# Kernel tuning notes

Hardware: AMD Instinct MI355X
Metric: run time of the kernel (lower is better)

Reference implementation:

```python
import jax, jax.numpy as jnp
import numpy as np

N = 200000   # total nodes across batched graphs
E = 800000   # directed edges (grid graph, avg degree ~4)
G = 8        # number of graphs in the batch
IN_DIM, INTER_DIM, OUT_DIM, LAYER_NUM = 2, 128, 64, 4


def setup_inputs() -> dict:
    key = jax.random.key(0)
    ks = jax.random.split(key, 10)
    x = jax.random.normal(ks[0], (N, IN_DIM), jnp.float32)
    edge_index = jax.random.randint(ks[1], (2, E), 0, N, dtype=jnp.int32)
    batch = jnp.sort(jax.random.randint(ks[2], (N,), 0, G, dtype=jnp.int32))

    def glorot(k, fan_in, fan_out):
        s = (2.0 / (fan_in + fan_out)) ** 0.5
        return jax.random.normal(k, (fan_in, fan_out), jnp.float32) * s

    W_in = glorot(ks[3], IN_DIM, INTER_DIM)
    b_in = jnp.zeros((INTER_DIM,), jnp.float32)
    W_hidden = jnp.stack([glorot(jax.random.fold_in(ks[4], i), INTER_DIM, INTER_DIM)
                          for i in range(LAYER_NUM)])
    b_hidden = jnp.zeros((LAYER_NUM, INTER_DIM), jnp.float32)
    W_out = glorot(ks[5], INTER_DIM, OUT_DIM)
    b_out = jnp.zeros((OUT_DIM,), jnp.float32)
    return {"x": x, "edge_index": edge_index, "batch": batch,
            "W_in": W_in, "b_in": b_in, "W_hidden": W_hidden,
            "b_hidden": b_hidden, "W_out": W_out, "b_out": b_out}


def reference(x, edge_index, batch, W_in, b_in, W_hidden, b_hidden, W_out, b_out):
    num_nodes = x.shape[0]
    loops = jnp.arange(num_nodes, dtype=edge_index.dtype)
    # PyG GCNConv: add self loops, symmetric degree normalization
    src = jnp.concatenate([edge_index[0], loops])
    dst = jnp.concatenate([edge_index[1], loops])
    deg = jax.ops.segment_sum(jnp.ones_like(src, x.dtype), dst, num_segments=num_nodes)
    dinv = jnp.where(deg > 0, jax.lax.rsqrt(jnp.maximum(deg, 1.0)), 0.0)
    norm = dinv[src] * dinv[dst]  # [E+N]

    def gcn_conv(h, W, b):
        m = h @ W                                  # [N, F'] dense transform
        msg = norm[:, None] * m[src]               # gather + scale
        out = jax.ops.segment_sum(msg, dst, num_segments=num_nodes)  # scatter-add
        return out + b

    h = gcn_conv(x, W_in, b_in)
    for i in range(W_hidden.shape[0]):
        h = jax.nn.relu(gcn_conv(h, W_hidden[i], b_hidden[i]))
    h = gcn_conv(h, W_out, b_out)

    # global mean pool over batch assignment, then sigmoid
    sums = jax.ops.segment_sum(h, batch, num_segments=G)
    cnts = jax.ops.segment_sum(jnp.ones((num_nodes,), h.dtype), batch, num_segments=G)
    return jax.nn.sigmoid(sums / jnp.maximum(cnts, 1.0)[:, None])
```

## Files before the change

kernel.cpp:

```cpp
#include <hip/hip_runtime.h>
#include <math.h>

#define INTER 128
#define OUTD  64
#define SCAN_T 256
#define SCAN_E 1024
#define NSLOT 64

using bf16x8 = __attribute__((ext_vector_type(8))) short;
using f32x4  = __attribute__((ext_vector_type(4))) float;

static __device__ __forceinline__ unsigned short f2bf(float f) {
    unsigned int u = __float_as_uint(f);
    u += 0x7fffu + ((u >> 16) & 1u);
    return (unsigned short)(u >> 16);
}
static __device__ __forceinline__ unsigned int pk2(float a, float b) {
    return (unsigned int)f2bf(a) | ((unsigned int)f2bf(b) << 16);
}
static __device__ __forceinline__ float bflo(unsigned int u) { return __uint_as_float(u << 16); }
static __device__ __forceinline__ float bfhi(unsigned int u) { return __uint_as_float(u & 0xffff0000u); }

static __device__ __forceinline__ void fma8(float* a, float w, uint4 v) {
    a[0] = fmaf(w, bflo(v.x), a[0]); a[1] = fmaf(w, bfhi(v.x), a[1]);
    a[2] = fmaf(w, bflo(v.y), a[2]); a[3] = fmaf(w, bfhi(v.y), a[3]);
    a[4] = fmaf(w, bflo(v.z), a[4]); a[5] = fmaf(w, bfhi(v.z), a[5]);
    a[6] = fmaf(w, bflo(v.w), a[6]); a[7] = fmaf(w, bfhi(v.w), a[7]);
}
static __device__ __forceinline__ void seed8(float* a, float sn, uint4 v) {
    a[0] = sn * bflo(v.x); a[1] = sn * bfhi(v.x);
    a[2] = sn * bflo(v.y); a[3] = sn * bfhi(v.y);
    a[4] = sn * bflo(v.z); a[5] = sn * bfhi(v.z);
    a[6] = sn * bflo(v.w); a[7] = sn * bfhi(v.w);
}
static __device__ __forceinline__ void seed4(float* a, float sn, uint2 v) {
    a[0] = sn * bflo(v.x); a[1] = sn * bfhi(v.x);
    a[2] = sn * bflo(v.y); a[3] = sn * bfhi(v.y);
}

__global__ void count_k(const int* __restrict__ dst, int* __restrict__ cnt, int E) {
    int e = blockIdx.x * 256 + threadIdx.x;
    if (e < E) atomicAdd(&cnt[dst[e]], 1);
}

__global__ void dinv_k(const int* __restrict__ cnt, float* __restrict__ dinv, int N) {
    int i = blockIdx.x * 256 + threadIdx.x;
    if (i < N) dinv[i] = rsqrtf((float)(cnt[i] + 1));
}

__global__ void scan_block(const int* __restrict__ in, int* __restrict__ out,
                           int* __restrict__ bsums, int n) {
    __shared__ int sh[SCAN_T];
    int base = blockIdx.x * SCAN_E;
    int t = threadIdx.x;
    int v[4];
    int s = 0;
#pragma unroll
    for (int i = 0; i < 4; i++) {
        int idx = base + t * 4 + i;
        v[i] = (idx < n) ? in[idx] : 0;
        s += v[i];
    }
    sh[t] = s;
    __syncthreads();
    for (int off = 1; off < SCAN_T; off <<= 1) {
        int x = (t >= off) ? sh[t - off] : 0;
        __syncthreads();
        sh[t] += x;
        __syncthreads();
    }
    int excl = (t == 0) ? 0 : sh[t - 1];
    if (bsums && t == SCAN_T - 1) bsums[blockIdx.x] = sh[t];
#pragma unroll
    for (int i = 0; i < 4; i++) {
        int idx = base + t * 4 + i;
        if (idx < n) out[idx] = excl;
        excl += v[i];
    }
}

__global__ void scan_add(int* __restrict__ out, const int* __restrict__ bsums, int n, int total) {
    int idx = blockIdx.x * SCAN_E + threadIdx.x * 4;
    int add = bsums[blockIdx.x];
#pragma unroll
    for (int i = 0; i < 4; i++) {
        int j = idx + i;
        if (j < n) out[j] += add;
    }
    if (blockIdx.x == 0 && threadIdx.x == 0) out[n] = total;
}

__global__ void scatter_k(const int* __restrict__ src, const int* __restrict__ dst,
                          const int* __restrict__ rs, int* __restrict__ cursor,
                          const float* __restrict__ dinv,
                          int2* __restrict__ cw, int E) {
    int e = blockIdx.x * 256 + threadIdx.x;
    if (e >= E) return;
    int s = src[e], d = dst[e];
    int pos = rs[d] + atomicAdd(&cursor[d], 1);
    cw[pos] = make_int2(s, __float_as_int(dinv[s] * dinv[d]));
}

__global__ void wprep_h(const float* __restrict__ W, unsigned short* __restrict__ Wt, int L) {
    int tid = blockIdx.x * 256 + threadIdx.x;
    if (tid >= L * INTER * INTER) return;
    int l = tid / (INTER * INTER);
    int r = tid % (INTER * INTER);
    int n = r / INTER, k = r % INTER;
    Wt[tid] = f2bf(W[(size_t)l * INTER * INTER + (size_t)k * INTER + n]);
}

__global__ void wprep_o(const float* __restrict__ W, unsigned short* __restrict__ Wt) {
    int tid = blockIdx.x * 256 + threadIdx.x;
    if (tid >= OUTD * INTER) return;
    int n = tid / INTER, k = tid % INTER;
    Wt[tid] = f2bf(W[(size_t)k * OUTD + n]);
}

__global__ void agg2(const float* __restrict__ x, const int* __restrict__ rs,
                     const int2* __restrict__ cw, const float* __restrict__ dinv,
                     float* __restrict__ ax, int N) {
    int i = blockIdx.x * 256 + threadIdx.x;
    if (i >= N) return;
    float di = dinv[i];
    float sn = di * di;
    float2 xv = ((const float2*)x)[i];
    float a0 = sn * xv.x, a1 = sn * xv.y;
    int e0 = rs[i], e1 = rs[i + 1];
    for (int k = e0; k < e1; k++) {
        int2 c = cw[k];
        float wk = __int_as_float(c.y);
        float2 xs = ((const float2*)x)[c.x];
        a0 += wk * xs.x;
        a1 += wk * xs.y;
    }
    ((float2*)ax)[i] = make_float2(a0, a1);
}

__global__ void gemm_in(const float* __restrict__ ax, const float* __restrict__ Wi,
                        const float* __restrict__ bi, unsigned short* __restrict__ h, int N) {
    int node = blockIdx.x * 2 + threadIdx.x / 128;
    int j = threadIdx.x % 128;
    if (node >= N) return;
    float2 a = ((const float2*)ax)[node];
    h[(size_t)node * 128 + j] = f2bf(fmaf(a.x, Wi[j], fmaf(a.y, Wi[128 + j], bi[j])));
}

__global__ __launch_bounds__(256) void fused_hidden2(
    const unsigned short* __restrict__ Hin,
    const int* __restrict__ rs, const int2* __restrict__ cw,
    const float* __restrict__ dinv,
    const unsigned short* __restrict__ Wt,
    const float* __restrict__ bias,
    unsigned short* __restrict__ Hout, int N)
{
    __shared__ __align__(16) unsigned short T[32][136];
    const int t = threadIdx.x;
    const int q = t & 15;
    const int gi = t >> 4;
    const int nA = blockIdx.x * 32 + gi;
    const int nB = nA + 16;
    const bool vA = nA < N, vB = nB < N;

    float accA[8] = {0,0,0,0,0,0,0,0}, accB[8] = {0,0,0,0,0,0,0,0};
    if (vA) {
        float dA = dinv[nA];
        seed8(accA, dA * dA, *(const uint4*)(Hin + (size_t)nA * 128 + q * 8));
    }
    if (vB) {
        float dB = dinv[nB];
        seed8(accB, dB * dB, *(const uint4*)(Hin + (size_t)nB * 128 + q * 8));
    }
    int kA = 0, eA = 0, kB = 0, eB = 0;
    if (vA) { kA = rs[nA]; eA = rs[nA + 1]; }
    if (vB) { kB = rs[nB]; eB = rs[nB + 1]; }

    while (kA < eA || kB < eB) {
        int2 cA0 = (kA     < eA) ? cw[kA]     : make_int2(0, 0);
        int2 cA1 = (kA + 1 < eA) ? cw[kA + 1] : make_int2(0, 0);
        int2 cA2 = (kA + 2 < eA) ? cw[kA + 2] : make_int2(0, 0);
        int2 cA3 = (kA + 3 < eA) ? cw[kA + 3] : make_int2(0, 0);
        int2 cB0 = (kB     < eB) ? cw[kB]     : make_int2(0, 0);
        int2 cB1 = (kB + 1 < eB) ? cw[kB + 1] : make_int2(0, 0);
        int2 cB2 = (kB + 2 < eB) ? cw[kB + 2] : make_int2(0, 0);
        int2 cB3 = (kB + 3 < eB) ? cw[kB + 3] : make_int2(0, 0);
        uint4 vA0 = *(const uint4*)(Hin + (size_t)cA0.x * 128 + q * 8);
        uint4 vA1 = *(const uint4*)(Hin + (size_t)cA1.x * 128 + q * 8);
        uint4 vA2 = *(const uint4*)(Hin + (size_t)cA2.x * 128 + q * 8);
        uint4 vA3 = *(const uint4*)(Hin + (size_t)cA3.x * 128 + q * 8);
        uint4 vB0 = *(const uint4*)(Hin + (size_t)cB0.x * 128 + q * 8);
        uint4 vB1 = *(const uint4*)(Hin + (size_t)cB1.x * 128 + q * 8);
        uint4 vB2 = *(const uint4*)(Hin + (size_t)cB2.x * 128 + q * 8);
        uint4 vB3 = *(const uint4*)(Hin + (size_t)cB3.x * 128 + q * 8);
        fma8(accA, __int_as_float(cA0.y), vA0);
        fma8(accA, __int_as_float(cA1.y), vA1);
        fma8(accA, __int_as_float(cA2.y), vA2);
        fma8(accA, __int_as_float(cA3.y), vA3);
        fma8(accB, __int_as_float(cB0.y), vB0);
        fma8(accB, __int_as_float(cB1.y), vB1);
        fma8(accB, __int_as_float(cB2.y), vB2);
        fma8(accB, __int_as_float(cB3.y), vB3);
        kA += 4; kB += 4;
    }

    {
        uint4 oA = make_uint4(pk2(accA[0], accA[1]), pk2(accA[2], accA[3]),
                              pk2(accA[4], accA[5]), pk2(accA[6], accA[7]));
        uint4 oB = make_uint4(pk2(accB[0], accB[1]), pk2(accB[2], accB[3]),
                              pk2(accB[4], accB[5]), pk2(accB[6], accB[7]));
        *(uint4*)&T[gi][q * 8] = oA;
        *(uint4*)&T[gi + 16][q * 8] = oB;
    }
    __syncthreads();

    const int wv = t >> 6;
    const int lane = t & 63;
    const int r15 = lane & 15;
    const int kg = lane >> 4;

    bf16x8 bfr[2][4];
#pragma unroll
    for (int nc = 0; nc < 2; nc++)
#pragma unroll
        for (int ks = 0; ks < 4; ks++)
            bfr[nc][ks] = *(const bf16x8*)&T[nc * 16 + r15][kg * 8 + ks * 32];

    f32x4 acc[2][2];
#pragma unroll
    for (int nc = 0; nc < 2; nc++)
#pragma unroll
        for (int c = 0; c < 2; c++) acc[nc][c] = (f32x4){0.f, 0.f, 0.f, 0.f};

#pragma unroll
    for (int c = 0; c < 2; c++) {
        const unsigned short* wrow = Wt + (size_t)(wv * 32 + c * 16 + r15) * 128 + kg * 8;
#pragma unroll
        for (int ks = 0; ks < 4; ks++) {
            bf16x8 afr = *(const bf16x8*)(wrow + ks * 32);
            acc[0][c] = __builtin_amdgcn_mfma_f32_16x16x32_bf16(afr, bfr[0][ks], acc[0][c], 0, 0, 0);
            acc[1][c] = __builtin_amdgcn_mfma_f32_16x16x32_bf16(afr, bfr[1][ks], acc[1][c], 0, 0, 0);
        }
    }

#pragma unroll
    for (int nc = 0; nc < 2; nc++) {
        const int node = blockIdx.x * 32 + nc * 16 + r15;
        if (node < N) {
#pragma unroll
            for (int c = 0; c < 2; c++) {
                int col = wv * 32 + c * 16 + kg * 4;
                float4 bv = *(const float4*)(bias + col);
                float v0 = fmaxf(acc[nc][c][0] + bv.x, 0.f);
                float v1 = fmaxf(acc[nc][c][1] + bv.y, 0.f);
                float v2 = fmaxf(acc[nc][c][2] + bv.z, 0.f);
                float v3 = fmaxf(acc[nc][c][3] + bv.w, 0.f);
                *(uint2*)(Hout + (size_t)node * 128 + col) = make_uint2(pk2(v0, v1), pk2(v2, v3));
            }
        }
    }
}

__global__ __launch_bounds__(256) void gemm_out(const unsigned short* __restrict__ Hin,
                                                const unsigned short* __restrict__ Wt,
                                                unsigned short* __restrict__ g, int N) {
    const int wv = threadIdx.x >> 6;
    const int lane = threadIdx.x & 63;
    const int r15 = lane & 15;
    const int kg = lane >> 4;
    const int node0 = blockIdx.x * 64 + wv * 16;
    if (node0 >= N) return;

    int arow = node0 + r15;
    if (arow >= N) arow = N - 1;
    bf16x8 bfr[4];
#pragma unroll
    for (int ks = 0; ks < 4; ks++)
        bfr[ks] = *(const bf16x8*)(Hin + (size_t)arow * 128 + kg * 8 + ks * 32);

    f32x4 acc[4];
#pragma unroll
    for (int c = 0; c < 4; c++) acc[c] = (f32x4){0.f, 0.f, 0.f, 0.f};

#pragma unroll
    for (int c = 0; c < 4; c++) {
        const unsigned short* wrow = Wt + (size_t)(c * 16 + r15) * 128 + kg * 8;
#pragma unroll
        for (int ks = 0; ks < 4; ks++) {
            bf16x8 afr = *(const bf16x8*)(wrow + ks * 32);
            acc[c] = __builtin_amdgcn_mfma_f32_16x16x32_bf16(afr, bfr[ks], acc[c], 0, 0, 0);
        }
    }
    const int node = node0 + r15;
    if (node < N) {
#pragma unroll
        for (int c = 0; c < 4; c++) {
            int col = c * 16 + kg * 4;
            *(uint2*)(g + (size_t)node * 64 + col) =
                make_uint2(pk2(acc[c][0], acc[c][1]), pk2(acc[c][2], acc[c][3]));
        }
    }
}

__global__ __launch_bounds__(256) void fused_last2(
    const unsigned short* __restrict__ g,
    const int* __restrict__ rs, const int2* __restrict__ cw,
    const float* __restrict__ dinv, const int* __restrict__ batch,
    float* __restrict__ gsum , int N)
{
    __shared__ __align__(16) float R[64][68];
    __shared__ int gid[64];
    const int t = threadIdx.x;
    const int q = t & 7;
    const int gi = t >> 3;
    const int nA = blockIdx.x * 64 + gi;
    const int nB = nA + 32;
    const bool vA = nA < N, vB = nB < N;

    float accA[8] = {0,0,0,0,0,0,0,0}, accB[8] = {0,0,0,0,0,0,0,0};
    if (vA) {
        float dA = dinv[nA];
        seed8(accA, dA * dA, *(const uint4*)(g + (size_t)nA * 64 + q * 8));
    }
    if (vB) {
        float dB = dinv[nB];
        seed8(accB, dB * dB, *(const uint4*)(g + (size_t)nB * 64 + q * 8));
    }
    int kA = 0, eA = 0, kB = 0, eB = 0;
    if (vA) { kA = rs[nA]; eA = rs[nA + 1]; }
    if (vB) { kB = rs[nB]; eB = rs[nB + 1]; }

    while (kA < eA || kB < eB) {
        int2 cA0 = (kA     < eA) ? cw[kA]     : make_int2(0, 0);
        int2 cA1 = (kA + 1 < eA) ? cw[kA + 1] : make_int2(0, 0);
        int2 cA2 = (kA + 2 < eA) ? cw[kA + 2] : make_int2(0, 0);
        int2 cA3 = (kA + 3 < eA) ? cw[kA + 3] : make_int2(0, 0);
        int2 cB0 = (kB     < eB) ? cw[kB]     : make_int2(0, 0);
        int2 cB1 = (kB + 1 < eB) ? cw[kB + 1] : make_int2(0, 0);
        int2 cB2 = (kB + 2 < eB) ? cw[kB + 2] : make_int2(0, 0);
        int2 cB3 = (kB + 3 < eB) ? cw[kB + 3] : make_int2(0, 0);
        uint4 vA0 = *(const uint4*)(g + (size_t)cA0.x * 64 + q * 8);
        uint4 vA1 = *(const uint4*)(g + (size_t)cA1.x * 64 + q * 8);
        uint4 vA2 = *(const uint4*)(g + (size_t)cA2.x * 64 + q * 8);
        uint4 vA3 = *(const uint4*)(g + (size_t)cA3.x * 64 + q * 8);
        uint4 vB0 = *(const uint4*)(g + (size_t)cB0.x * 64 + q * 8);
        uint4 vB1 = *(const uint4*)(g + (size_t)cB1.x * 64 + q * 8);
        uint4 vB2 = *(const uint4*)(g + (size_t)cB2.x * 64 + q * 8);
        uint4 vB3 = *(const uint4*)(g + (size_t)cB3.x * 64 + q * 8);
        fma8(accA, __int_as_float(cA0.y), vA0);
        fma8(accA, __int_as_float(cA1.y), vA1);
        fma8(accA, __int_as_float(cA2.y), vA2);
        fma8(accA, __int_as_float(cA3.y), vA3);
        fma8(accB, __int_as_float(cB0.y), vB0);
        fma8(accB, __int_as_float(cB1.y), vB1);
        fma8(accB, __int_as_float(cB2.y), vB2);
        fma8(accB, __int_as_float(cB3.y), vB3);
        kA += 4; kB += 4;
    }

#pragma unroll
    for (int j = 0; j < 8; j += 4) {
        *(float4*)&R[gi][q * 8 + j]      = make_float4(accA[j], accA[j+1], accA[j+2], accA[j+3]);
        *(float4*)&R[gi + 32][q * 8 + j] = make_float4(accB[j], accB[j+1], accB[j+2], accB[j+3]);
    }
    if (q == 0) {
        gid[gi]      = vA ? batch[nA] : -1;
        gid[gi + 32] = vB ? batch[nB] : -1;
    }
    __syncthreads();

    const int f = t & 63;
    const int half = t >> 6;
    const int slot = blockIdx.x & (NSLOT - 1);
    float acc = 0.f;
    int cur = -1;
    for (int r = 0; r < 16; r++) {
        int row = half * 16 + r;
        int gg = gid[row];
        if (gg != cur) {
            if (cur >= 0) atomicAdd(&gsum[(size_t)(slot * 8 + cur) * 64 + f], acc);
            acc = 0.f; cur = gg;
        }
        if (gg >= 0) acc += R[row][f];
    }
    if (cur >= 0) atomicAdd(&gsum[(size_t)(slot * 8 + cur) * 64 + f], acc);
}

__global__ void gbound_k(const int* __restrict__ batch, int* __restrict__ gstart, int N, int G) {
    int i = blockIdx.x * 256 + threadIdx.x;
    if (i >= N) return;
    int b = batch[i];
    int prev = (i == 0) ? -1 : batch[i - 1];
    for (int g = prev + 1; g <= b; g++) gstart[g] = i;
    if (i == N - 1) for (int g = b + 1; g <= G; g++) gstart[g] = N;
}

__global__ void final4_k(const float* __restrict__ gsum, const int* __restrict__ gstart,
                         const float* __restrict__ b_out, float* __restrict__ out) {
    int t = threadIdx.x;
    int g = t >> 6, f = t & 63;
    float s = 0.f;
    for (int sl = 0; sl < NSLOT; sl++) s += gsum[(size_t)(sl * 8 + g) * 64 + f];
    int c = gstart[g + 1] - gstart[g];
    float v = s / (float)max(c, 1) + b_out[f];
    out[g * 64 + f] = 1.f / (1.f + expf(-v));
}

extern "C" void kernel_launch(void* const* d_in, const int* in_sizes, int n_in,
                              void* d_out, int out_size, void* d_ws, size_t ws_size,
                              hipStream_t stream) {
    const float* x     = (const float*)d_in[0];
    const int*   ei    = (const int*)d_in[1];
    const int*   batch = (const int*)d_in[2];
    const float* W_in  = (const float*)d_in[3];
    const float* b_in  = (const float*)d_in[4];
    const float* W_h   = (const float*)d_in[5];
    const float* b_h   = (const float*)d_in[6];
    const float* W_out = (const float*)d_in[7];
    const float* b_out = (const float*)d_in[8];

    const int N = in_sizes[2];
    const int E = in_sizes[1] / 2;
    const int L = in_sizes[5] / (INTER * INTER);
    const int G = 8;
    const int* src = ei;
    const int* dst = ei + E;

    char* ws = (char*)d_ws;
    size_t off = 0;
    auto alloc = [&](size_t bytes) -> void* {
        void* p = ws + off;
        off += (bytes + 255) & ~(size_t)255;
        return p;
    };
    int*   cnt    = (int*)alloc((size_t)N * 4);
    int*   cursor = (int*)alloc((size_t)N * 4);
    int*   rs     = (int*)alloc((size_t)(N + 1) * 4);
    int*   bsums  = (int*)alloc(4096);
    float* dinv   = (float*)alloc((size_t)N * 4);
    int2*  cw     = (int2*)alloc((size_t)E * 8);
    float* ax     = (float*)alloc((size_t)N * 2 * 4);
    unsigned short* h   = (unsigned short*)alloc((size_t)N * INTER * 2);
    unsigned short* h2  = (unsigned short*)alloc((size_t)N * INTER * 2);
    unsigned short* g   = (unsigned short*)alloc((size_t)N * OUTD * 2);
    unsigned short* Wht = (unsigned short*)alloc((size_t)L * INTER * INTER * 2);
    unsigned short* Wot = (unsigned short*)alloc((size_t)OUTD * INTER * 2);
    float* gsum   = (float*)alloc((size_t)NSLOT * 8 * OUTD * 4);
    int*   gstart = (int*)alloc((G + 1) * 4);
    (void)ws_size; (void)n_in;

    hipMemsetAsync(cnt, 0, (size_t)N * 4, stream);
    hipMemsetAsync(cursor, 0, (size_t)N * 4, stream);
    hipMemsetAsync(gsum, 0, (size_t)NSLOT * 8 * OUTD * 4, stream);

    count_k<<<(E + 255) / 256, 256, 0, stream>>>(dst, cnt, E);
    dinv_k<<<(N + 255) / 256, 256, 0, stream>>>(cnt, dinv, N);
    int nsb = (N + SCAN_E - 1) / SCAN_E;
    scan_block<<<nsb, SCAN_T, 0, stream>>>(cnt, rs, bsums, N);
    scan_block<<<1, SCAN_T, 0, stream>>>(bsums, bsums, nullptr, nsb);
    scan_add<<<nsb, SCAN_T, 0, stream>>>(rs, bsums, N, E);
    scatter_k<<<(E + 255) / 256, 256, 0, stream>>>(src, dst, rs, cursor, dinv, cw, E);
    gbound_k<<<(N + 255) / 256, 256, 0, stream>>>(batch, gstart, N, G);

    wprep_h<<<(L * INTER * INTER + 255) / 256, 256, 0, stream>>>(W_h, Wht, L);
    wprep_o<<<(OUTD * INTER + 255) / 256, 256, 0, stream>>>(W_out, Wot);

    agg2<<<(N + 255) / 256, 256, 0, stream>>>(x, rs, cw, dinv, ax, N);
    gemm_in<<<(N + 1) / 2, 256, 0, stream>>>(ax, W_in, b_in, h, N);

    unsigned short* hin = h;
    unsigned short* hout = h2;
    for (int l = 0; l < L; l++) {
        fused_hidden2<<<(N + 31) / 32, 256, 0, stream>>>(
            hin, rs, cw, dinv, Wht + (size_t)l * INTER * INTER, b_h + (size_t)l * INTER, hout, N);
        unsigned short* tmp = hin; hin = hout; hout = tmp;
    }

    gemm_out<<<(N + 63) / 64, 256, 0, stream>>>(hin, Wot, g, N);
    fused_last2<<<(N + 63) / 64, 256, 0, stream>>>(g, rs, cw, dinv, batch, gsum, N);
    final4_k<<<1, 512, 0, stream>>>(gsum, gstart, b_out, (float*)d_out);
}
```

Before: 564.2 us.

## Use one node per thread group with 512-thread blocks in hidden layers

The fused hidden-layer kernel now runs 512 threads per block for the same 32-node tile. Each 16-lane group aggregates a single node, with the edge loop unrolled by 8 instead of interleaving two nodes by 4. The MFMA stage splits into 8 waves that each compute a 16-column slice rather than 4 waves covering 32 columns. Hidden outputs are written with nontemporal stores and gemm_out reads its input with nontemporal loads. The intent is more parallel gather threads and more in-flight memory requests per node, in exchange for more waves per block and more lanes idling on padded edges.

```diff
diff --git a/kernel.cpp b/kernel.cpp
--- a/kernel.cpp
+++ b/kernel.cpp
@@ -32,10 +32,6 @@
     a[2] = sn * bflo(v.y); a[3] = sn * bfhi(v.y);
     a[4] = sn * bflo(v.z); a[5] = sn * bfhi(v.z);
     a[6] = sn * bflo(v.w); a[7] = sn * bfhi(v.w);
-}
-static __device__ __forceinline__ void seed4(float* a, float sn, uint2 v) {
-    a[0] = sn * bflo(v.x); a[1] = sn * bfhi(v.x);
-    a[2] = sn * bflo(v.y); a[3] = sn * bfhi(v.y);
 }
 
 __global__ void count_k(const int* __restrict__ dst, int* __restrict__ cnt, int E) {
@@ -146,7 +142,7 @@
     h[(size_t)node * 128 + j] = f2bf(fmaf(a.x, Wi[j], fmaf(a.y, Wi[128 + j], bi[j])));
 }
 
-__global__ __launch_bounds__(256) void fused_hidden2(
+__global__ __launch_bounds__(512) void fused_hidden3(
     const unsigned short* __restrict__ Hin,
     const int* __restrict__ rs, const int2* __restrict__ cw,
     const float* __restrict__ dinv,
@@ -158,59 +154,46 @@
     const int t = threadIdx.x;
     const int q = t & 15;
     const int gi = t >> 4;
-    const int nA = blockIdx.x * 32 + gi;
-    const int nB = nA + 16;
-    const bool vA = nA < N, vB = nB < N;
-
-    float accA[8] = {0,0,0,0,0,0,0,0}, accB[8] = {0,0,0,0,0,0,0,0};
-    if (vA) {
-        float dA = dinv[nA];
-        seed8(accA, dA * dA, *(const uint4*)(Hin + (size_t)nA * 128 + q * 8));
-    }
-    if (vB) {
-        float dB = dinv[nB];
-        seed8(accB, dB * dB, *(const uint4*)(Hin + (size_t)nB * 128 + q * 8));
-    }
-    int kA = 0, eA = 0, kB = 0, eB = 0;
-    if (vA) { kA = rs[nA]; eA = rs[nA + 1]; }
-    if (vB) { kB = rs[nB]; eB = rs[nB + 1]; }
-
-    while (kA < eA || kB < eB) {
-        int2 cA0 = (kA     < eA) ? cw[kA]     : make_int2(0, 0);
-        int2 cA1 = (kA + 1 < eA) ? cw[kA + 1] : make_int2(0, 0);
-        int2 cA2 = (kA + 2 < eA) ? cw[kA + 2] : make_int2(0, 0);
-        int2 cA3 = (kA + 3 < eA) ? cw[kA + 3] : make_int2(0, 0);
-        int2 cB0 = (kB     < eB) ? cw[kB]     : make_int2(0, 0);
-        int2 cB1 = (kB + 1 < eB) ? cw[kB + 1] : make_int2(0, 0);
-        int2 cB2 = (kB + 2 < eB) ? cw[kB + 2] : make_int2(0, 0);
-        int2 cB3 = (kB + 3 < eB) ? cw[kB + 3] : make_int2(0, 0);
-        uint4 vA0 = *(const uint4*)(Hin + (size_t)cA0.x * 128 + q * 8);
-        uint4 vA1 = *(const uint4*)(Hin + (size_t)cA1.x * 128 + q * 8);
-        uint4 vA2 = *(const uint4*)(Hin + (size_t)cA2.x * 128 + q * 8);
-        uint4 vA3 = *(const uint4*)(Hin + (size_t)cA3.x * 128 + q * 8);
-        uint4 vB0 = *(const uint4*)(Hin + (size_t)cB0.x * 128 + q * 8);
-        uint4 vB1 = *(const uint4*)(Hin + (size_t)cB1.x * 128 + q * 8);
-        uint4 vB2 = *(const uint4*)(Hin + (size_t)cB2.x * 128 + q * 8);
-        uint4 vB3 = *(const uint4*)(Hin + (size_t)cB3.x * 128 + q * 8);
-        fma8(accA, __int_as_float(cA0.y), vA0);
-        fma8(accA, __int_as_float(cA1.y), vA1);
-        fma8(accA, __int_as_float(cA2.y), vA2);
-        fma8(accA, __int_as_float(cA3.y), vA3);
-        fma8(accB, __int_as_float(cB0.y), vB0);
-        fma8(accB, __int_as_float(cB1.y), vB1);
-        fma8(accB, __int_as_float(cB2.y), vB2);
-        fma8(accB, __int_as_float(cB3.y), vB3);
-        kA += 4; kB += 4;
-    }
-
-    {
-        uint4 oA = make_uint4(pk2(accA[0], accA[1]), pk2(accA[2], accA[3]),
-                              pk2(accA[4], accA[5]), pk2(accA[6], accA[7]));
-        uint4 oB = make_uint4(pk2(accB[0], accB[1]), pk2(accB[2], accB[3]),
-                              pk2(accB[4], accB[5]), pk2(accB[6], accB[7]));
-        *(uint4*)&T[gi][q * 8] = oA;
-        *(uint4*)&T[gi + 16][q * 8] = oB;
-    }
+    const int n = blockIdx.x * 32 + gi;
+    const bool vn = n < N;
+
+    float acc[8] = {0,0,0,0,0,0,0,0};
+    int k0 = 0, e0 = 0;
+    if (vn) {
+        float d = dinv[n];
+        seed8(acc, d * d, *(const uint4*)(Hin + (size_t)n * 128 + q * 8));
+        k0 = rs[n]; e0 = rs[n + 1];
+    }
+
+    for (int k = k0; k < e0; k += 8) {
+        int2 c0 = (k     < e0) ? cw[k]     : make_int2(0, 0);
+        int2 c1 = (k + 1 < e0) ? cw[k + 1] : make_int2(0, 0);
+        int2 c2 = (k + 2 < e0) ? cw[k + 2] : make_int2(0, 0);
+        int2 c3 = (k + 3 < e0) ? cw[k + 3] : make_int2(0, 0);
+        int2 c4 = (k + 4 < e0) ? cw[k + 4] : make_int2(0, 0);
+        int2 c5 = (k + 5 < e0) ? cw[k + 5] : make_int2(0, 0);
+        int2 c6 = (k + 6 < e0) ? cw[k + 6] : make_int2(0, 0);
+        int2 c7 = (k + 7 < e0) ? cw[k + 7] : make_int2(0, 0);
+        uint4 v0 = *(const uint4*)(Hin + (size_t)c0.x * 128 + q * 8);
+        uint4 v1 = *(const uint4*)(Hin + (size_t)c1.x * 128 + q * 8);
+        uint4 v2 = *(const uint4*)(Hin + (size_t)c2.x * 128 + q * 8);
+        uint4 v3 = *(const uint4*)(Hin + (size_t)c3.x * 128 + q * 8);
+        uint4 v4 = *(const uint4*)(Hin + (size_t)c4.x * 128 + q * 8);
+        uint4 v5 = *(const uint4*)(Hin + (size_t)c5.x * 128 + q * 8);
+        uint4 v6 = *(const uint4*)(Hin + (size_t)c6.x * 128 + q * 8);
+        uint4 v7 = *(const uint4*)(Hin + (size_t)c7.x * 128 + q * 8);
+        fma8(acc, __int_as_float(c0.y), v0);
+        fma8(acc, __int_as_float(c1.y), v1);
+        fma8(acc, __int_as_float(c2.y), v2);
+        fma8(acc, __int_as_float(c3.y), v3);
+        fma8(acc, __int_as_float(c4.y), v4);
+        fma8(acc, __int_as_float(c5.y), v5);
+        fma8(acc, __int_as_float(c6.y), v6);
+        fma8(acc, __int_as_float(c7.y), v7);
+    }
+
+    *(uint4*)&T[gi][q * 8] = make_uint4(pk2(acc[0], acc[1]), pk2(acc[2], acc[3]),
+                                        pk2(acc[4], acc[5]), pk2(acc[6], acc[7]));
     __syncthreads();
 
     const int wv = t >> 6;
@@ -225,37 +208,31 @@
         for (int ks = 0; ks < 4; ks++)
             bfr[nc][ks] = *(const bf16x8*)&T[nc * 16 + r15][kg * 8 + ks * 32];
 
-    f32x4 acc[2][2];
-#pragma unroll
-    for (int nc = 0; nc < 2; nc++)
-#pragma unroll
-        for (int c = 0; c < 2; c++) acc[nc][c] = (f32x4){0.f, 0.f, 0.f, 0.f};
-
-#pragma unroll
-    for (int c = 0; c < 2; c++) {
-        const unsigned short* wrow = Wt + (size_t)(wv * 32 + c * 16 + r15) * 128 + kg * 8;
-#pragma unroll
-        for (int ks = 0; ks < 4; ks++) {
-            bf16x8 afr = *(const bf16x8*)(wrow + ks * 32);
-            acc[0][c] = __builtin_amdgcn_mfma_f32_16x16x32_bf16(afr, bfr[0][ks], acc[0][c], 0, 0, 0);
-            acc[1][c] = __builtin_amdgcn_mfma_f32_16x16x32_bf16(afr, bfr[1][ks], acc[1][c], 0, 0, 0);
-        }
-    }
-
+    f32x4 a2[2];
+    a2[0] = (f32x4){0.f, 0.f, 0.f, 0.f};
+    a2[1] = (f32x4){0.f, 0.f, 0.f, 0.f};
+
+    const unsigned short* wrow = Wt + (size_t)(wv * 16 + r15) * 128 + kg * 8;
+#pragma unroll
+    for (int ks = 0; ks < 4; ks++) {
+        bf16x8 afr = *(const bf16x8*)(wrow + ks * 32);
+        a2[0] = __builtin_amdgcn_mfma_f32_16x16x32_bf16(afr, bfr[0][ks], a2[0], 0, 0, 0);
+        a2[1] = __builtin_amdgcn_mfma_f32_16x16x32_bf16(afr, bfr[1][ks], a2[1], 0, 0, 0);
+    }
+
+    const int col = wv * 16 + kg * 4;
+    const float4 bv = *(const float4*)(bias + col);
 #pragma unroll
     for (int nc = 0; nc < 2; nc++) {
         const int node = blockIdx.x * 32 + nc * 16 + r15;
         if (node < N) {
-#pragma unroll
-            for (int c = 0; c < 2; c++) {
-                int col = wv * 32 + c * 16 + kg * 4;
-                float4 bv = *(const float4*)(bias + col);
-                float v0 = fmaxf(acc[nc][c][0] + bv.x, 0.f);
-                float v1 = fmaxf(acc[nc][c][1] + bv.y, 0.f);
-                float v2 = fmaxf(acc[nc][c][2] + bv.z, 0.f);
-                float v3 = fmaxf(acc[nc][c][3] + bv.w, 0.f);
-                *(uint2*)(Hout + (size_t)node * 128 + col) = make_uint2(pk2(v0, v1), pk2(v2, v3));
-            }
+            float v0 = fmaxf(a2[nc][0] + bv.x, 0.f);
+            float v1 = fmaxf(a2[nc][1] + bv.y, 0.f);
+            float v2 = fmaxf(a2[nc][2] + bv.z, 0.f);
+            float v3 = fmaxf(a2[nc][3] + bv.w, 0.f);
+            unsigned long long pkd = (unsigned long long)pk2(v0, v1)
+                                   | ((unsigned long long)pk2(v2, v3) << 32);
+            __builtin_nontemporal_store(pkd, (unsigned long long*)(Hout + (size_t)node * 128 + col));
         }
     }
 }
@@ -275,7 +252,8 @@
     bf16x8 bfr[4];
 #pragma unroll
     for (int ks = 0; ks < 4; ks++)
-        bfr[ks] = *(const bf16x8*)(Hin + (size_t)arow * 128 + kg * 8 + ks * 32);
+        bfr[ks] = __builtin_nontemporal_load(
+            (const bf16x8*)(Hin + (size_t)arow * 128 + kg * 8 + ks * 32));
 
     f32x4 acc[4];
 #pragma unroll
@@ -470,7 +448,7 @@
     unsigned short* hin = h;
     unsigned short* hout = h2;
     for (int l = 0; l < L; l++) {
-        fused_hidden2<<<(N + 31) / 32, 256, 0, stream>>>(
+        fused_hidden3<<<(N + 31) / 32, 512, 0, stream>>>(
             hin, rs, cw, dinv, Wht + (size_t)l * INTER * INTER, b_h + (size_t)l * INTER, hout, N);
         unsigned short* tmp = hin; hin = hout; hout = tmp;
     }
```

New measurement: 585.9 us. 1.04x slower.

## Process hidden-layer nodes in degree-sorted order to balance per-block work

Applied to the files above, without the earlier changes.

Adds a counting sort of nodes by in-degree (histogram, scan, scatter into an order array). The fused hidden-layer kernel then processes nodes in that order, so each 32-node block handles nodes of similar degree and waits less on its slowest node. The cost is three small extra kernels and scattered row reads and writes, because neighbouring nodes in a block are no longer contiguous in memory. A nontemporal load hint is also added in gemm_out.

```diff
diff --git a/kernel.cpp b/kernel.cpp
--- a/kernel.cpp
+++ b/kernel.cpp
@@ -6,6 +6,7 @@
 #define SCAN_T 256
 #define SCAN_E 1024
 #define NSLOT 64
+#define NBIN  128
 
 using bf16x8 = __attribute__((ext_vector_type(8))) short;
 using f32x4  = __attribute__((ext_vector_type(4))) float;
@@ -32,10 +33,6 @@
     a[2] = sn * bflo(v.y); a[3] = sn * bfhi(v.y);
     a[4] = sn * bflo(v.z); a[5] = sn * bfhi(v.z);
     a[6] = sn * bflo(v.w); a[7] = sn * bfhi(v.w);
-}
-static __device__ __forceinline__ void seed4(float* a, float sn, uint2 v) {
-    a[0] = sn * bflo(v.x); a[1] = sn * bfhi(v.x);
-    a[2] = sn * bflo(v.y); a[3] = sn * bfhi(v.y);
 }
 
 __global__ void count_k(const int* __restrict__ dst, int* __restrict__ cnt, int E) {
@@ -99,6 +96,27 @@
     int s = src[e], d = dst[e];
     int pos = rs[d] + atomicAdd(&cursor[d], 1);
     cw[pos] = make_int2(s, __float_as_int(dinv[s] * dinv[d]));
+}
+
+__global__ void dhist_k(const int* __restrict__ cnt, int* __restrict__ hist, int N) {
+    int i = blockIdx.x * 256 + threadIdx.x;
+    if (i < N) atomicAdd(&hist[min(cnt[i], NBIN - 1)], 1);
+}
+
+__global__ void dscan_k(const int* __restrict__ hist, int* __restrict__ bincur) {
+    if (threadIdx.x == 0) {
+        int s = 0;
+        for (int b = 0; b < NBIN; b++) { bincur[b] = s; s += hist[b]; }
+    }
+}
+
+__global__ void dorder_k(const int* __restrict__ cnt, int* __restrict__ bincur,
+                         int* __restrict__ order, int N) {
+    int i = blockIdx.x * 256 + threadIdx.x;
+    if (i >= N) return;
+    int d = min(cnt[i], NBIN - 1);
+    int p = atomicAdd(&bincur[d], 1);
+    order[p] = i;
 }
 
 __global__ void wprep_h(const float* __restrict__ W, unsigned short* __restrict__ Wt, int L) {
@@ -146,21 +164,28 @@
     h[(size_t)node * 128 + j] = f2bf(fmaf(a.x, Wi[j], fmaf(a.y, Wi[128 + j], bi[j])));
 }
 
-__global__ __launch_bounds__(256) void fused_hidden2(
+__global__ __launch_bounds__(256) void fused_hidden4(
     const unsigned short* __restrict__ Hin,
     const int* __restrict__ rs, const int2* __restrict__ cw,
-    const float* __restrict__ dinv,
+    const float* __restrict__ dinv, const int* __restrict__ order,
     const unsigned short* __restrict__ Wt,
     const float* __restrict__ bias,
     unsigned short* __restrict__ Hout, int N)
 {
     __shared__ __align__(16) unsigned short T[32][136];
+    __shared__ int nodeid[32];
     const int t = threadIdx.x;
     const int q = t & 15;
     const int gi = t >> 4;
-    const int nA = blockIdx.x * 32 + gi;
-    const int nB = nA + 16;
-    const bool vA = nA < N, vB = nB < N;
+    const int sA = blockIdx.x * 32 + gi;
+    const int sB = sA + 16;
+    const bool vA = sA < N, vB = sB < N;
+    const int nA = vA ? order[sA] : 0;
+    const int nB = vB ? order[sB] : 0;
+    if (q == 0) {
+        nodeid[gi]      = vA ? nA : -1;
+        nodeid[gi + 16] = vB ? nB : -1;
+    }
 
     float accA[8] = {0,0,0,0,0,0,0,0}, accB[8] = {0,0,0,0,0,0,0,0};
     if (vA) {
@@ -244,8 +269,8 @@
 
 #pragma unroll
     for (int nc = 0; nc < 2; nc++) {
-        const int node = blockIdx.x * 32 + nc * 16 + r15;
-        if (node < N) {
+        const int node = nodeid[nc * 16 + r15];
+        if (node >= 0) {
 #pragma unroll
             for (int c = 0; c < 2; c++) {
                 int col = wv * 32 + c * 16 + kg * 4;
@@ -275,7 +300,8 @@
     bf16x8 bfr[4];
 #pragma unroll
     for (int ks = 0; ks < 4; ks++)
-        bfr[ks] = *(const bf16x8*)(Hin + (size_t)arow * 128 + kg * 8 + ks * 32);
+        bfr[ks] = __builtin_nontemporal_load(
+            (const bf16x8*)(Hin + (size_t)arow * 128 + kg * 8 + ks * 32));
 
     f32x4 acc[4];
 #pragma unroll
@@ -446,11 +472,15 @@
     unsigned short* Wot = (unsigned short*)alloc((size_t)OUTD * INTER * 2);
     float* gsum   = (float*)alloc((size_t)NSLOT * 8 * OUTD * 4);
     int*   gstart = (int*)alloc((G + 1) * 4);
+    int*   hist   = (int*)alloc(NBIN * 4);
+    int*   bincur = (int*)alloc(NBIN * 4);
+    int*   order  = (int*)alloc((size_t)N * 4);
     (void)ws_size; (void)n_in;
 
     hipMemsetAsync(cnt, 0, (size_t)N * 4, stream);
     hipMemsetAsync(cursor, 0, (size_t)N * 4, stream);
     hipMemsetAsync(gsum, 0, (size_t)NSLOT * 8 * OUTD * 4, stream);
+    hipMemsetAsync(hist, 0, NBIN * 4, stream);
 
     count_k<<<(E + 255) / 256, 256, 0, stream>>>(dst, cnt, E);
     dinv_k<<<(N + 255) / 256, 256, 0, stream>>>(cnt, dinv, N);
@@ -461,6 +491,10 @@
     scatter_k<<<(E + 255) / 256, 256, 0, stream>>>(src, dst, rs, cursor, dinv, cw, E);
     gbound_k<<<(N + 255) / 256, 256, 0, stream>>>(batch, gstart, N, G);
 
+    dhist_k<<<(N + 255) / 256, 256, 0, stream>>>(cnt, hist, N);
+    dscan_k<<<1, 64, 0, stream>>>(hist, bincur);
+    dorder_k<<<(N + 255) / 256, 256, 0, stream>>>(cnt, bincur, order, N);
+
     wprep_h<<<(L * INTER * INTER + 255) / 256, 256, 0, stream>>>(W_h, Wht, L);
     wprep_o<<<(OUTD * INTER + 255) / 256, 256, 0, stream>>>(W_out, Wot);
 
@@ -470,8 +504,8 @@
     unsigned short* hin = h;
     unsigned short* hout = h2;
     for (int l = 0; l < L; l++) {
-        fused_hidden2<<<(N + 31) / 32, 256, 0, stream>>>(
-            hin, rs, cw, dinv, Wht + (size_t)l * INTER * INTER, b_h + (size_t)l * INTER, hout, N);
+        fused_hidden4<<<(N + 31) / 32, 256, 0, stream>>>(
+            hin, rs, cw, dinv, order, Wht + (size_t)l * INTER * INTER, b_h + (size_t)l * INTER, hout, N);
         unsigned short* tmp = hin; hin = hout; hout = tmp;
     }
 
```

After: 2.174 ms. +285.4%, slower.
